# Optimization experiments

Hardware: AMD Instinct MI355X
Metric: run time of the kernel (lower is better)

## Reference

```python
import jax, jax.numpy as jnp
import numpy as np

N_NODES = 100000
N_EDGES = 800000
D_IN = 100
D_HID = 100
N_CLS = 16


def setup_inputs() -> dict:
    key = jax.random.key(0)
    ks = jax.random.split(key, 7)
    x = jax.random.normal(ks[0], (N_NODES, D_IN), dtype=jnp.float32)
    edge_index = jax.random.randint(ks[1], (2, N_EDGES), 0, N_NODES, dtype=jnp.int64)
    s = 1.0 / np.sqrt(D_IN)
    Wl = jax.random.normal(ks[2], (D_HID, D_IN), dtype=jnp.float32) * s
    bl = jax.random.normal(ks[3], (D_HID,), dtype=jnp.float32) * s
    Wr = jax.random.normal(ks[4], (D_HID, D_IN), dtype=jnp.float32) * s
    sc = 1.0 / np.sqrt(D_HID)
    Wc = jax.random.normal(ks[5], (N_CLS, D_HID), dtype=jnp.float32) * sc
    bc = jax.random.normal(ks[6], (N_CLS,), dtype=jnp.float32) * sc
    return {"x": x, "edge_index": edge_index, "Wl": Wl, "bl": bl,
            "Wr": Wr, "Wc": Wc, "bc": bc}


def reference(x, edge_index, Wl, bl, Wr, Wc, bc):
    # SAGEConv (mean aggregation): out_i = Wl @ mean_{j in N(i)} x_j + bl + Wr @ x_i
    src, dst = edge_index[0], edge_index[1]
    n = x.shape[0]
    agg = jax.ops.segment_sum(x[src], dst, num_segments=n)          # [N, D_IN]
    deg = jax.ops.segment_sum(jnp.ones((src.shape[0],), x.dtype), dst, num_segments=n)
    mean = agg / jnp.maximum(deg, 1.0)[:, None]
    h = mean @ Wl.T + bl + x @ Wr.T                                  # [N, D_HID]
    h = jax.nn.relu(h)
    out = h @ Wc.T + bc                                              # [N, N_CLS]
    return out
```

## Files before the change

### kernel.cpp

```cpp
#include <hip/hip_runtime.h>
#include <hip/hip_bf16.h>
#include <hip/hip_fp16.h>

#define N_NODES 100000
#define N_EDGES 800000
#define D_IN 100
#define D_HID 100
#define N_CLS 16

#define TN 64
#define SK 232
#define AK 200
#define SCHUNK 1024
#define SNBLK 98

typedef _Float16 f16x8 __attribute__((ext_vector_type(8)));
typedef _Float16 f16x4 __attribute__((ext_vector_type(4)));
typedef float f32x4 __attribute__((ext_vector_type(4)));

__global__ __launch_bounds__(256) void hist_k(const int* __restrict__ ei,
                                              int* __restrict__ cnt)
{
    const int e = blockIdx.x * 256 + threadIdx.x;
    if (e < N_EDGES) atomicAdd(&cnt[ei[N_EDGES + e]], 1);
}

__global__ __launch_bounds__(256) void scan_a(const int* __restrict__ cnt,
                                              int* __restrict__ bsum)
{
    __shared__ int red[256];
    const int t = threadIdx.x;
    const int base = blockIdx.x * SCHUNK + t * 4;
    int s = 0;
    if (base + 3 < N_NODES) {
        const int4 v = *reinterpret_cast<const int4*>(cnt + base);
        s = v.x + v.y + v.z + v.w;
    } else {
        for (int i = 0; i < 4; ++i)
            if (base + i < N_NODES) s += cnt[base + i];
    }
    red[t] = s;
    __syncthreads();
    for (int d = 128; d > 0; d >>= 1) {
        if (t < d) red[t] += red[t + d];
        __syncthreads();
    }
    if (t == 0) bsum[blockIdx.x] = red[0];
}

__global__ __launch_bounds__(128) void scan_b(const int* __restrict__ bsum,
                                              int* __restrict__ boffs)
{
    __shared__ int s[128];
    const int t = threadIdx.x;
    const int v = (t < SNBLK) ? bsum[t] : 0;
    s[t] = v;
    __syncthreads();
    for (int d = 1; d < 128; d <<= 1) {
        const int a = s[t];
        const int add = (t >= d) ? s[t - d] : 0;
        __syncthreads();
        s[t] = a + add;
        __syncthreads();
    }
    if (t < SNBLK) boffs[t] = s[t] - v;
}

__global__ __launch_bounds__(256) void scan_c(const int* __restrict__ cnt,
                                              const int* __restrict__ boffs,
                                              int* __restrict__ wofs)
{
    __shared__ int red[256];
    const int t = threadIdx.x;
    const int base = blockIdx.x * SCHUNK + t * 4;
    int c0 = 0, c1 = 0, c2 = 0, c3 = 0;
    if (base + 3 < N_NODES) {
        const int4 v = *reinterpret_cast<const int4*>(cnt + base);
        c0 = v.x; c1 = v.y; c2 = v.z; c3 = v.w;
    } else {
        if (base + 0 < N_NODES) c0 = cnt[base + 0];
        if (base + 1 < N_NODES) c1 = cnt[base + 1];
        if (base + 2 < N_NODES) c2 = cnt[base + 2];
        if (base + 3 < N_NODES) c3 = cnt[base + 3];
    }
    const int s = c0 + c1 + c2 + c3;
    red[t] = s;
    __syncthreads();
    for (int d = 1; d < 256; d <<= 1) {
        const int a = red[t];
        const int add = (t >= d) ? red[t - d] : 0;
        __syncthreads();
        red[t] = a + add;
        __syncthreads();
    }
    int prefix = boffs[blockIdx.x] + red[t] - s;
    const int c[4] = {c0, c1, c2, c3};
    for (int i = 0; i < 4; ++i) {
        const int idx = base + i;
        if (idx < N_NODES) {
            wofs[idx] = prefix;
            prefix += c[i];
        }
    }
}

__global__ __launch_bounds__(256) void fill_csr(const int* __restrict__ ei,
                                                int* __restrict__ wofs,
                                                int* __restrict__ esrc)
{
    const int e = blockIdx.x * 256 + threadIdx.x;
    if (e >= N_EDGES) return;
    const int src = ei[e];
    const int dst = ei[N_EDGES + e];
    const int pos = atomicAdd(&wofs[dst], 1);
    esrc[pos] = src;
}

__global__ __launch_bounds__(256) void cvt_w16(const float* __restrict__ Wl,
                                               const float* __restrict__ Wr,
                                               _Float16* __restrict__ w16)
{
    const int idx = blockIdx.x * 256 + threadIdx.x;
    if (idx >= 128 * 58) return;
    const int o = idx / 58, s = idx - o * 58;
    const int k0 = s * 4;
    float4 v = make_float4(0.f, 0.f, 0.f, 0.f);
    if (o < 100) {
        if (s < 25)       v = *reinterpret_cast<const float4*>(Wl + o * 100 + k0);
        else if (s < 50)  v = *reinterpret_cast<const float4*>(Wr + o * 100 + (k0 - 100));
    }
    f16x4 h = { (_Float16)v.x, (_Float16)v.y, (_Float16)v.z, (_Float16)v.w };
    *reinterpret_cast<f16x4*>(w16 + o * SK + k0) = h;
}

__global__ __launch_bounds__(256) void cvt_x16(const float* __restrict__ x,
                                               _Float16* __restrict__ amx)
{
    const int idx = blockIdx.x * 256 + threadIdx.x;
    if (idx >= N_NODES * 25) return;
    const int n = idx / 25, s = idx - n * 25;
    const float4 v = *reinterpret_cast<const float4*>(x + (long)n * D_IN + s * 4);
    f16x4 h = { (_Float16)v.x, (_Float16)v.y, (_Float16)v.z, (_Float16)v.w };
    *reinterpret_cast<f16x4*>(amx + (long)n * AK + 100 + s * 4) = h;
}

__global__ __launch_bounds__(256) void gather_mean(
    const int* __restrict__ wofs, const int* __restrict__ esrc,
    _Float16* __restrict__ amx)
{
    const int node = blockIdx.x * 8 + (threadIdx.x >> 5);
    if (node >= N_NODES) return;
    const int l = threadIdx.x & 31;
    const int r0 = (node == 0) ? 0 : wofs[node - 1];
    const int r1 = wofs[node];
    const int deg = r1 - r0;

    float4 acc = make_float4(0.f, 0.f, 0.f, 0.f);
    for (int base = 0; base < deg; base += 32) {
        int s = 0;
        if (base + l < deg) s = esrc[r0 + base + l];
        const int rem = deg - base;
        const int m = rem < 32 ? rem : 32;
        for (int j = 0; j < m; ++j) {
            const int src = __shfl(s, j, 32);
            if (l < 25) {
                const f16x4 v = *reinterpret_cast<const f16x4*>(
                    amx + (long)src * AK + 100 + l * 4);
                acc.x += (float)v[0]; acc.y += (float)v[1];
                acc.z += (float)v[2]; acc.w += (float)v[3];
            }
        }
    }
    if (l < 25) {
        const float inv = 1.0f / fmaxf((float)deg, 1.0f);
        f16x4 h = { (_Float16)(acc.x * inv), (_Float16)(acc.y * inv),
                    (_Float16)(acc.z * inv), (_Float16)(acc.w * inv) };
        *reinterpret_cast<f16x4*>(amx + (long)node * AK + l * 4) = h;
    }
}

__global__ __launch_bounds__(512, 1) void sage_node(
    const _Float16* __restrict__ amx, const _Float16* __restrict__ w16,
    const float* __restrict__ bl, const float* __restrict__ Wc,
    const float* __restrict__ bc, float* __restrict__ out)
{
    __shared__ __align__(16) _Float16 wS[128 * SK];
    __shared__ __align__(16) _Float16 aS[TN * SK];
    __shared__ float wcS[16 * 100];
    __shared__ float blS[128];
    __shared__ float bcS[16];

    const int tid = threadIdx.x;
    const int wid = tid >> 6;
    const int lane = tid & 63;
    const int node0 = blockIdx.x * TN;

    for (int c = tid; c < 128 * 29; c += 512) {
        const f16x8 v = *reinterpret_cast<const f16x8*>(w16 + c * 8);
        *reinterpret_cast<f16x8*>(wS + c * 8) = v;
    }
    {
        const f16x8 z = { (_Float16)0.f, (_Float16)0.f, (_Float16)0.f, (_Float16)0.f,
                          (_Float16)0.f, (_Float16)0.f, (_Float16)0.f, (_Float16)0.f };
        const _Float16* ga = amx + (size_t)node0 * AK;
        for (int c = tid; c < 64 * 29; c += 512) {
            const int row = c / 29, j = c - row * 29;
            f16x8 v = z;
            if (j < 25) v = *reinterpret_cast<const f16x8*>(ga + row * AK + j * 8);
            *reinterpret_cast<f16x8*>(aS + row * SK + j * 8) = v;
        }
    }
    for (int i = tid; i < 1600; i += 512) wcS[i] = Wc[i];
    if (tid < 128) blS[tid] = (tid < 100) ? bl[tid] : 0.0f;
    if (tid < 16)  bcS[tid] = bc[tid];
    __syncthreads();

    const int wr = wid >> 2;
    const int wq = wid & 3;
    const int lrow = lane & 15;
    const int lk = (lane >> 4) * 8;

    f32x4 acc00 = {0.f, 0.f, 0.f, 0.f}, acc01 = acc00, acc10 = acc00, acc11 = acc00;
    const _Float16* aB = aS + (wr * 32 + lrow) * SK + lk;
    const _Float16* bB = wS + (wq * 32 + lrow) * SK + lk;

    #pragma unroll
    for (int ks = 0; ks < 7; ++ks) {
        const f16x8 a0 = *reinterpret_cast<const f16x8*>(aB + ks * 32);
        const f16x8 a1 = *reinterpret_cast<const f16x8*>(aB + 16 * SK + ks * 32);
        const f16x8 b0 = *reinterpret_cast<const f16x8*>(bB + ks * 32);
        const f16x8 b1 = *reinterpret_cast<const f16x8*>(bB + 16 * SK + ks * 32);
        acc00 = __builtin_amdgcn_mfma_f32_16x16x32_f16(a0, b0, acc00, 0, 0, 0);
        acc01 = __builtin_amdgcn_mfma_f32_16x16x32_f16(a0, b1, acc01, 0, 0, 0);
        acc10 = __builtin_amdgcn_mfma_f32_16x16x32_f16(a1, b0, acc10, 0, 0, 0);
        acc11 = __builtin_amdgcn_mfma_f32_16x16x32_f16(a1, b1, acc11, 0, 0, 0);
    }
    __syncthreads();

    float* hS = reinterpret_cast<float*>(wS);
    const int crow = (lane >> 4) * 4;
    const int ccol = lane & 15;
    #pragma unroll
    for (int mi = 0; mi < 2; ++mi) {
        #pragma unroll
        for (int ni = 0; ni < 2; ++ni) {
            const f32x4 a = (mi == 0) ? (ni == 0 ? acc00 : acc01)
                                      : (ni == 0 ? acc10 : acc11);
            const int o = wq * 32 + ni * 16 + ccol;
            #pragma unroll
            for (int r = 0; r < 4; ++r) {
                const int nl = wr * 32 + mi * 16 + crow + r;
                if (o < 104)
                    hS[nl * 104 + o] = fmaxf(a[r] + blS[o], 0.0f);
            }
        }
    }
    __syncthreads();

    {
        const int nl = tid >> 3;
        const int q = tid & 7;
        float o0 = bcS[2 * q], o1 = bcS[2 * q + 1];
        const float* hP = hS + nl * 104;
        const float* w0 = wcS + (2 * q) * 100;
        const float* w1 = wcS + (2 * q + 1) * 100;
        for (int o = 0; o < 100; o += 4) {
            const float4 h4 = *reinterpret_cast<const float4*>(hP + o);
            const float4 a = *reinterpret_cast<const float4*>(w0 + o);
            const float4 b = *reinterpret_cast<const float4*>(w1 + o);
            o0 += h4.x * a.x + h4.y * a.y + h4.z * a.z + h4.w * a.w;
            o1 += h4.x * b.x + h4.y * b.y + h4.z * b.z + h4.w * b.w;
        }
        const int node = node0 + nl;
        if (node < N_NODES)
            *reinterpret_cast<float2*>(out + (long)node * N_CLS + 2 * q) =
                make_float2(o0, o1);
    }
}

extern "C" void kernel_launch(void* const* d_in, const int* in_sizes, int n_in,
                              void* d_out, int out_size, void* d_ws, size_t ws_size,
                              hipStream_t stream) {
    const float* x  = (const float*)d_in[0];
    const int*   ei = (const int*)d_in[1];
    const float* Wl = (const float*)d_in[2];
    const float* bl = (const float*)d_in[3];
    const float* Wr = (const float*)d_in[4];
    const float* Wc = (const float*)d_in[5];
    const float* bc = (const float*)d_in[6];
    float* out = (float*)d_out;

    int* cnt    = (int*)d_ws;
    int* wofs   = cnt + N_NODES;
    int* esrc   = wofs + N_NODES + 4;
    int* bsum   = esrc + N_EDGES;
    int* boffs  = bsum + 128;
    _Float16* w16 = (_Float16*)(boffs + 128);
    _Float16* amx = w16 + 128 * SK;

    hipMemsetAsync(cnt, 0, N_NODES * sizeof(int), stream);

    hist_k<<<(N_EDGES + 255) / 256, 256, 0, stream>>>(ei, cnt);
    scan_a<<<SNBLK, 256, 0, stream>>>(cnt, bsum);
    scan_b<<<1, 128, 0, stream>>>(bsum, boffs);
    scan_c<<<SNBLK, 256, 0, stream>>>(cnt, boffs, wofs);
    fill_csr<<<(N_EDGES + 255) / 256, 256, 0, stream>>>(ei, wofs, esrc);
    cvt_w16<<<(128 * 58 + 255) / 256, 256, 0, stream>>>(Wl, Wr, w16);
    cvt_x16<<<(N_NODES * 25 + 255) / 256, 256, 0, stream>>>(x, amx);
    gather_mean<<<(N_NODES + 7) / 8, 256, 0, stream>>>(wofs, esrc, amx);

    sage_node<<<(N_NODES + TN - 1) / TN, 512, 0, stream>>>(
        amx, w16, bl, Wc, bc, out);
}
```

Baseline: 277.7 us.

## Record per-edge rank in histogram to drop fill atomics and merge scan kernels

The histogram pass now stores the atomicAdd return value as a 16-bit rank per edge. The CSR fill then computes positions as exclusive offset plus rank, with no second atomic. The separate block-offset scan kernel is folded into scan_c, which removes one launch, and wofs becomes a true exclusive prefix with a sentinel at N_NODES. The rank buffer reuses the unused slots of the amx feature area before cvt_x16 overwrites them, so correctness depends on that aliasing and on degrees fitting in 16 bits.

```diff
diff --git a/kernel.cpp b/kernel.cpp
--- a/kernel.cpp
+++ b/kernel.cpp
@@ -18,11 +18,18 @@
 typedef _Float16 f16x4 __attribute__((ext_vector_type(4)));
 typedef float f32x4 __attribute__((ext_vector_type(4)));
 
+#define RANK_SLOT(e) (((e) >> 7) * AK + ((e) & 127))
+
 __global__ __launch_bounds__(256) void hist_k(const int* __restrict__ ei,
-                                              int* __restrict__ cnt)
+                                              int* __restrict__ cnt,
+                                              unsigned short* __restrict__ rank16)
 {
     const int e = blockIdx.x * 256 + threadIdx.x;
-    if (e < N_EDGES) atomicAdd(&cnt[ei[N_EDGES + e]], 1);
+    if (e < N_EDGES) {
+        const int dst = ei[N_EDGES + e];
+        const int r = atomicAdd(&cnt[dst], 1);
+        rank16[RANK_SLOT(e)] = (unsigned short)r;
+    }
 }
 
 __global__ __launch_bounds__(256) void scan_a(const int* __restrict__ cnt,
@@ -48,30 +55,25 @@
     if (t == 0) bsum[blockIdx.x] = red[0];
 }
 
-__global__ __launch_bounds__(128) void scan_b(const int* __restrict__ bsum,
-                                              int* __restrict__ boffs)
-{
-    __shared__ int s[128];
+__global__ __launch_bounds__(256) void scan_c(const int* __restrict__ cnt,
+                                              const int* __restrict__ bsum,
+                                              int* __restrict__ wofs)
+{
+    __shared__ int red[256];
+    __shared__ int sb[128];
     const int t = threadIdx.x;
-    const int v = (t < SNBLK) ? bsum[t] : 0;
-    s[t] = v;
+    if (t < 128) sb[t] = (t < SNBLK) ? bsum[t] : 0;
     __syncthreads();
     for (int d = 1; d < 128; d <<= 1) {
-        const int a = s[t];
-        const int add = (t >= d) ? s[t - d] : 0;
-        __syncthreads();
-        s[t] = a + add;
-        __syncthreads();
-    }
-    if (t < SNBLK) boffs[t] = s[t] - v;
-}
-
-__global__ __launch_bounds__(256) void scan_c(const int* __restrict__ cnt,
-                                              const int* __restrict__ boffs,
-                                              int* __restrict__ wofs)
-{
-    __shared__ int red[256];
-    const int t = threadIdx.x;
+        int a = 0;
+        if (t < 128) { a = sb[t]; if (t >= d) a += sb[t - d]; }
+        __syncthreads();
+        if (t < 128) sb[t] = a;
+        __syncthreads();
+    }
+    const int bofs = sb[blockIdx.x] - bsum[blockIdx.x];
+    if (blockIdx.x == 0 && t == 0) wofs[N_NODES] = sb[SNBLK - 1];
+
     const int base = blockIdx.x * SCHUNK + t * 4;
     int c0 = 0, c1 = 0, c2 = 0, c3 = 0;
     if (base + 3 < N_NODES) {
@@ -93,7 +95,7 @@
         red[t] = a + add;
         __syncthreads();
     }
-    int prefix = boffs[blockIdx.x] + red[t] - s;
+    int prefix = bofs + red[t] - s;
     const int c[4] = {c0, c1, c2, c3};
     for (int i = 0; i < 4; ++i) {
         const int idx = base + i;
@@ -105,14 +107,15 @@
 }
 
 __global__ __launch_bounds__(256) void fill_csr(const int* __restrict__ ei,
-                                                int* __restrict__ wofs,
+                                                const int* __restrict__ wofs,
+                                                const unsigned short* __restrict__ rank16,
                                                 int* __restrict__ esrc)
 {
     const int e = blockIdx.x * 256 + threadIdx.x;
     if (e >= N_EDGES) return;
     const int src = ei[e];
     const int dst = ei[N_EDGES + e];
-    const int pos = atomicAdd(&wofs[dst], 1);
+    const int pos = wofs[dst] + (int)rank16[RANK_SLOT(e)];
     esrc[pos] = src;
 }
 
@@ -151,8 +154,8 @@
     const int node = blockIdx.x * 8 + (threadIdx.x >> 5);
     if (node >= N_NODES) return;
     const int l = threadIdx.x & 31;
-    const int r0 = (node == 0) ? 0 : wofs[node - 1];
-    const int r1 = wofs[node];
+    const int r0 = wofs[node];
+    const int r1 = wofs[node + 1];
     const int deg = r1 - r0;
 
     float4 acc = make_float4(0.f, 0.f, 0.f, 0.f);
@@ -294,17 +297,16 @@
     int* wofs   = cnt + N_NODES;
     int* esrc   = wofs + N_NODES + 4;
     int* bsum   = esrc + N_EDGES;
-    int* boffs  = bsum + 128;
-    _Float16* w16 = (_Float16*)(boffs + 128);
+    _Float16* w16 = (_Float16*)(bsum + 128);
     _Float16* amx = w16 + 128 * SK;
+    unsigned short* rank16 = (unsigned short*)amx;
 
     hipMemsetAsync(cnt, 0, N_NODES * sizeof(int), stream);
 
-    hist_k<<<(N_EDGES + 255) / 256, 256, 0, stream>>>(ei, cnt);
+    hist_k<<<(N_EDGES + 255) / 256, 256, 0, stream>>>(ei, cnt, rank16);
     scan_a<<<SNBLK, 256, 0, stream>>>(cnt, bsum);
-    scan_b<<<1, 128, 0, stream>>>(bsum, boffs);
-    scan_c<<<SNBLK, 256, 0, stream>>>(cnt, boffs, wofs);
-    fill_csr<<<(N_EDGES + 255) / 256, 256, 0, stream>>>(ei, wofs, esrc);
+    scan_c<<<SNBLK, 256, 0, stream>>>(cnt, bsum, wofs);
+    fill_csr<<<(N_EDGES + 255) / 256, 256, 0, stream>>>(ei, wofs, rank16, esrc);
     cvt_w16<<<(128 * 58 + 255) / 256, 256, 0, stream>>>(Wl, Wr, w16);
     cvt_x16<<<(N_NODES * 25 + 255) / 256, 256, 0, stream>>>(x, amx);
     gather_mean<<<(N_NODES + 7) / 8, 256, 0, stream>>>(wofs, esrc, amx);
```

New measurement: 240.8 us. 13.3% less time.
